# Performance work log

Measured on AMD Instinct MI355X. Metric: run time of the kernel, lower is better.

## Reference

```python
import jax, jax.numpy as jnp
import numpy as np

N = 4_194_304
B = 64
H = 16
TAU = 1.0


def setup_inputs() -> dict:
    key = jax.random.key(0)
    ks = jax.random.split(key, 8)
    pos = jax.random.normal(ks[0], (N, 3), dtype=jnp.float32)
    reflectance = jax.random.uniform(ks[1], (N,), dtype=jnp.float32)
    batch = jnp.sort(jax.random.randint(ks[2], (N,), 0, B).astype(jnp.int32))
    gumbels = jax.random.gumbel(ks[3], (B, 2), dtype=jnp.float32)
    W1 = jax.random.normal(ks[4], (4, H), dtype=jnp.float32) * 0.5
    b1 = jnp.zeros((H,), dtype=jnp.float32)
    W2 = jax.random.normal(ks[5], (H, H), dtype=jnp.float32) * 0.25
    b2 = jnp.zeros((H,), dtype=jnp.float32)
    Wg = jax.random.normal(ks[6], (H, 2), dtype=jnp.float32) * 0.25
    bg = jnp.array([0.0, 2.0], dtype=jnp.float32)  # gate_nn bias init per module
    return {"pos": pos, "reflectance": reflectance, "batch": batch, "gumbels": gumbels,
            "W1": W1, "b1": b1, "W2": W2, "b2": b2, "Wg": Wg, "bg": bg}


def reference(pos, reflectance, batch, gumbels, W1, b1, W2, b2, Wg, bg):
    # point-wise MLP: [N,4] -> [N,H]
    features = jnp.concatenate([pos, reflectance[:, None]], axis=-1)
    h = jax.nn.relu(features @ W1 + b1)
    h = jax.nn.relu(h @ W2 + b2)
    # batch-indexed max pool: [N,H] -> [B,H]
    sample_features = jax.ops.segment_max(h, batch, num_segments=B)
    gate_logits = sample_features @ Wg + bg  # [B,2]
    # gumbel-softmax (hard=False as in forward)
    gate_decision = jax.nn.softmax((gate_logits + gumbels) / TAU, axis=-1)
    # gather per-point gate and scale reflectance
    use_reflectance = gate_decision[:, 1][batch]  # [N]
    return use_reflectance * reflectance
```

## Files before the change

kernel.cpp:

```cpp
#include <hip/hip_runtime.h>
#include <hip/hip_bf16.h>


#define N_PTS 4194304
#define NB 64
#define NH 16
#define WPB 4
#define SITERS 2
#define PTW (256 * SITERS)
#define PPB (WPB * PTW)
#define NBLK (N_PTS / PPB)
#define NENT (NBLK * 2)

typedef __attribute__((ext_vector_type(8))) short bf16x8;
typedef __attribute__((ext_vector_type(4))) float f32x4;
union U8 { bf16x8 v; unsigned u[4]; unsigned short s[8]; };

struct Rec { int idA, idB, bpos; };
struct F3  { float x, y, z; };

__device__ __forceinline__ unsigned pk2(float a, float b) {
    float2 t; t.x = a; t.y = b;
    __hip_bfloat162 r = __float22bfloat162_rn(t);
    unsigned u;
    __builtin_memcpy(&u, &r, sizeof(u));
    return u;
}
__device__ __forceinline__ unsigned short f2bf(float x) {
    unsigned u = __float_as_uint(x);
    u = u + 0x7fffu + ((u >> 16) & 1u);
    return (unsigned short)(u >> 16);
}

template<bool SLOW>
__device__ __forceinline__ void do_chunk(
    const F3 p[4], const float4& rv,
    int sb, int g, int col, int bposw,
    const U8& A1, const U8& A2, const f32x4& c1, const f32x4& c2,
    f32x4& accA, f32x4& accB)
{
    const float f[4][4] = {{p[0].x, p[0].y, p[0].z, rv.x},
                           {p[1].x, p[1].y, p[1].z, rv.y},
                           {p[2].x, p[2].y, p[2].z, rv.z},
                           {p[3].x, p[3].y, p[3].z, rv.w}};
#pragma unroll
    for (int j = 0; j < 4; ++j) {
        const unsigned F01 = pk2(f[j][0], f[j][1]);
        const unsigned F23 = pk2(f[j][2], f[j][3]);
        f32x4 d[4], h[4];
#pragma unroll
        for (int t = 0; t < 4; ++t) {
            const bool mine = (g == t);
            U8 B;
            B.u[0] = mine ? F01 : 0u;
            B.u[1] = mine ? F23 : 0u;
            B.u[2] = 0u; B.u[3] = 0u;
            d[t] = __builtin_amdgcn_mfma_f32_16x16x32_bf16(A1.v, B.v, c1, 0, 0, 0);
        }
#pragma unroll
        for (int t = 0; t < 4; ++t) {
            U8 P;
            P.u[0] = pk2(fmaxf(d[t][0], 0.f), fmaxf(d[t][1], 0.f));
            P.u[1] = pk2(fmaxf(d[t][2], 0.f), fmaxf(d[t][3], 0.f));
            P.u[2] = 0u; P.u[3] = 0u;
            h[t] = __builtin_amdgcn_mfma_f32_16x16x32_bf16(A2.v, P.v, c2, 0, 0, 0);
        }
#pragma unroll
        for (int t = 0; t < 4; ++t) {
            if (!SLOW) {
#pragma unroll
                for (int r = 0; r < 4; ++r) accA[r] = fmaxf(accA[r], h[t][r]);
            } else {
                const bool m = (sb + 64 * j + 16 * t + col) < bposw;
#pragma unroll
                for (int r = 0; r < 4; ++r) {
                    accA[r] = fmaxf(accA[r], m ? h[t][r] : 0.f);
                    accB[r] = fmaxf(accB[r], m ? 0.f : h[t][r]);
                }
            }
        }
    }
}

__global__ __launch_bounds__(256, 8) void mlp_segmax_kernel(
    const float* __restrict__ pos,
    const float* __restrict__ refl,
    const int*   __restrict__ batch,
    const float* __restrict__ W1, const float* __restrict__ b1,
    const float* __restrict__ W2, const float* __restrict__ b2,
    float* __restrict__ pv,
    int*   __restrict__ pid,
    Rec*   __restrict__ recs)
{
    __shared__ float wlds[352];
    __shared__ float lv[WPB][2][NH];
    __shared__ int   li[WPB][2];
    __shared__ int   lbp[WPB];

    const int tid  = threadIdx.x;
    const int lane = tid & 63;
    const int wid  = tid >> 6;
    const int col  = lane & 15;
    const int g    = lane >> 4;
    const int wb   = (blockIdx.x * WPB + wid) * PTW;

    if (tid < 64)  wlds[tid]        = W1[tid];
    if (tid < 16)  wlds[64 + tid]   = b1[tid];
    wlds[80 + tid] = W2[tid];
    if (tid < 16)  wlds[336 + tid]  = b2[tid];
    __syncthreads();

    U8 A1, A2;
#pragma unroll
    for (int e = 0; e < 4; ++e) {
        A1.s[e]     = f2bf(wlds[e * NH + col]);
        A1.s[e + 4] = 0;
        A2.s[e]     = f2bf(wlds[80 + (4 * g + e) * NH + col]);
        A2.s[e + 4] = 0;
    }
    f32x4 c1, c2;
#pragma unroll
    for (int r = 0; r < 4; ++r) {
        c1[r] = wlds[64 + 4 * g + r];
        c2[r] = wlds[336 + 4 * g + r];
    }

    const int idA = batch[wb];
    const int idB = batch[wb + PTW - 1];
    const bool isSlow = (idA != idB);

    f32x4 accA = {0.f, 0.f, 0.f, 0.f};
    f32x4 accB = {0.f, 0.f, 0.f, 0.f};

    if (!isSlow) {
#pragma unroll
        for (int s = 0; s < SITERS; ++s) {
            const int sb = wb + s * 256;
            const float* pb = pos + (size_t)sb * 3;
            const float* rb = refl + sb;
            F3 p[4];
            __builtin_memcpy(&p[0], pb + 3 * (0 * 64 + lane), 12);
            __builtin_memcpy(&p[1], pb + 3 * (1 * 64 + lane), 12);
            __builtin_memcpy(&p[2], pb + 3 * (2 * 64 + lane), 12);
            __builtin_memcpy(&p[3], pb + 3 * (3 * 64 + lane), 12);
            float4 rv;
            rv.x = rb[0 * 64 + lane];
            rv.y = rb[1 * 64 + lane];
            rv.z = rb[2 * 64 + lane];
            rv.w = rb[3 * 64 + lane];
            do_chunk<false>(p, rv, sb, g, col, 0,
                            A1, A2, c1, c2, accA, accB);
        }
    } else {
        int bposw = 0x7fffffff;
        for (int it = 0; it < PTW / 64; ++it) {
            const int idx = wb + it * 64 + lane;
            const unsigned long long mk = __ballot(batch[idx] != idA);
            if (mk) bposw = min(bposw, wb + it * 64 + (__ffsll((long long)mk) - 1));
        }
#pragma unroll
        for (int s = 0; s < SITERS; ++s) {
            const int sb = wb + s * 256;
            const float* pb = pos + (size_t)sb * 3;
            const float* rb = refl + sb;
            F3 p[4];
            __builtin_memcpy(&p[0], pb + 3 * (0 * 64 + lane), 12);
            __builtin_memcpy(&p[1], pb + 3 * (1 * 64 + lane), 12);
            __builtin_memcpy(&p[2], pb + 3 * (2 * 64 + lane), 12);
            __builtin_memcpy(&p[3], pb + 3 * (3 * 64 + lane), 12);
            float4 rv;
            rv.x = rb[0 * 64 + lane];
            rv.y = rb[1 * 64 + lane];
            rv.z = rb[2 * 64 + lane];
            rv.w = rb[3 * 64 + lane];
            do_chunk<true>(p, rv, sb, g, col, bposw,
                           A1, A2, c1, c2, accA, accB);
        }
        lbp[wid] = bposw;
    }

#pragma unroll
    for (int mk = 1; mk <= 8; mk <<= 1) {
#pragma unroll
        for (int r = 0; r < 4; ++r) {
            accA[r] = fmaxf(accA[r], __shfl_xor(accA[r], mk));
            accB[r] = fmaxf(accB[r], __shfl_xor(accB[r], mk));
        }
    }
    if (col == 0) {
        *reinterpret_cast<float4*>(&lv[wid][0][4 * g]) =
            make_float4(accA[0], accA[1], accA[2], accA[3]);
        *reinterpret_cast<float4*>(&lv[wid][1][4 * g]) =
            make_float4(accB[0], accB[1], accB[2], accB[3]);
    }
    if (lane == 0) {
        li[wid][0] = idA; li[wid][1] = idB;
        if (!isSlow) lbp[wid] = 0x7fffffff;
    }
    __syncthreads();

    if (tid < NH) {
        const int d   = tid;
        const int ida = li[0][0];
        const int idb = li[WPB - 1][1];
        float mA = 0.f, mB = 0.f;
#pragma unroll
        for (int s = 0; s < WPB; ++s)
#pragma unroll
            for (int hh = 0; hh < 2; ++hh) {
                const float val = lv[s][hh][d];
                if (li[s][hh] == ida) mA = fmaxf(mA, val);
                else                  mB = fmaxf(mB, val);
            }
        pv[(blockIdx.x * 2 + 0) * NH + d] = mA;
        pv[(blockIdx.x * 2 + 1) * NH + d] = mB;
        if (d == 0) {
            pid[blockIdx.x * 2 + 0] = ida;
            pid[blockIdx.x * 2 + 1] = idb;
            int bp = 0x7fffffff;
#pragma unroll
            for (int s = 0; s < WPB; ++s) {
                if (li[s][0] != ida) bp = min(bp, (int)(blockIdx.x * PPB + s * PTW));
                else if (lbp[s] != 0x7fffffff) bp = min(bp, lbp[s]);
            }
            Rec r; r.idA = ida; r.idB = idb; r.bpos = bp;
            recs[blockIdx.x] = r;
        }
    }
}

__global__ __launch_bounds__(256) void gate_scale_kernel(
    const float* __restrict__ refl,
    const float* __restrict__ pv,
    const int*   __restrict__ pid,
    const Rec*   __restrict__ recs,
    const float* __restrict__ Wg, const float* __restrict__ bg,
    const float* __restrict__ gum,
    float* __restrict__ out)
{
    __shared__ unsigned smA[NH], smB[NH];
    __shared__ unsigned short list[256];
    __shared__ unsigned cnt;
    __shared__ float gAB[2];

    const int tid = threadIdx.x;
    const Rec rec = recs[blockIdx.x >> 1];

    if (tid < NH) { smA[tid] = 0u; smB[tid] = 0u; }
    if (tid == 0) cnt = 0u;
    __syncthreads();

#pragma unroll
    for (int k = 0; k < NENT / 256; ++k) {
        const int e = k * 256 + tid;
        const int p = pid[e];
        const bool a = (p == rec.idA);
        const bool b = (p == rec.idB) && !a;
        if (a || b) {
            const unsigned i = atomicAdd(&cnt, 1u);
            if (i < 256u) list[i] = (unsigned short)(e | (a ? 0 : 0x8000));
        }
    }
    __syncthreads();

    const int n = (int)(cnt < 256u ? cnt : 256u);
    for (int k = tid; k < n * NH; k += 256) {
        const int i = k >> 4, d = k & 15;
        const int e = list[i] & 0x7fff;
        unsigned* dst = (list[i] & 0x8000) ? smB : smA;
        atomicMax(dst + d, __float_as_uint(pv[e * NH + d]));
    }
    __syncthreads();

    if (tid < 2) {
        const int bsel = tid ? rec.idB : rec.idA;
        const unsigned* sm = tid ? smB : smA;
        float l0 = bg[0] + gum[bsel * 2 + 0];
        float l1 = bg[1] + gum[bsel * 2 + 1];
#pragma unroll
        for (int k = 0; k < NH; ++k) {
            const float s = __uint_as_float(sm[k]);
            l0 = fmaf(s, Wg[k * 2 + 0], l0);
            l1 = fmaf(s, Wg[k * 2 + 1], l1);
        }
        gAB[tid] = 1.f / (1.f + expf(-(l1 - l0)));
    }
    __syncthreads();

    const float gA = gAB[0];
    const float gB = (rec.idA == rec.idB) ? gAB[0] : gAB[1];

    const int p0 = (blockIdx.x * 256 + tid) * 4;
    const float4 rv = *reinterpret_cast<const float4*>(refl + p0);
    float4 o;
    o.x = ((p0 + 0) < rec.bpos ? gA : gB) * rv.x;
    o.y = ((p0 + 1) < rec.bpos ? gA : gB) * rv.y;
    o.z = ((p0 + 2) < rec.bpos ? gA : gB) * rv.z;
    o.w = ((p0 + 3) < rec.bpos ? gA : gB) * rv.w;
    *reinterpret_cast<float4*>(out + p0) = o;
}

extern "C" void kernel_launch(void* const* d_in, const int* in_sizes, int n_in,
                              void* d_out, int out_size, void* d_ws, size_t ws_size,
                              hipStream_t stream) {
    const float* pos   = (const float*)d_in[0];
    const float* refl  = (const float*)d_in[1];
    const int*   batch = (const int*)d_in[2];
    const float* gumb  = (const float*)d_in[3];
    const float* W1    = (const float*)d_in[4];
    const float* b1    = (const float*)d_in[5];
    const float* W2    = (const float*)d_in[6];
    const float* b2    = (const float*)d_in[7];
    const float* Wg    = (const float*)d_in[8];
    const float* bg    = (const float*)d_in[9];
    float* out = (float*)d_out;

    float* pv   = (float*)d_ws;
    int*   pid  = (int*)((char*)d_ws + 262144);
    Rec*   recs = (Rec*)((char*)d_ws + 278528);

    mlp_segmax_kernel<<<NBLK, 256, 0, stream>>>(pos, refl, batch,
                                                W1, b1, W2, b2, pv, pid, recs);
    gate_scale_kernel<<<N_PTS / 1024, 256, 0, stream>>>(refl, pv, pid, recs,
                                                        Wg, bg, gumb, out);
}
```

Before: 43.17 us.

## Halve points per MLP block and have each gate block cover two MLP records

The MLP/segment-max kernel now processes 256 points per wavefront instead of 512, which doubles its grid to 4096 blocks and the partial-max entries to 8192. The gate/scale kernel now handles 2048 points per block, merging two consecutive block records and recomputing the segment boundary, and its list capacity grows to 384. The intent is more parallelism in the first kernel, at the cost of the gate kernel scanning twice as many partial entries per block. Workspace offsets are moved to fit the larger partial arrays.

```diff
diff --git a/kernel.cpp b/kernel.cpp
--- a/kernel.cpp
+++ b/kernel.cpp
@@ -6,11 +6,13 @@
 #define NB 64
 #define NH 16
 #define WPB 4
-#define SITERS 2
+#define SITERS 1
 #define PTW (256 * SITERS)
 #define PPB (WPB * PTW)
 #define NBLK (N_PTS / PPB)
 #define NENT (NBLK * 2)
+#define BPPB 2048
+#define NBBLK (N_PTS / BPPB)
 
 typedef __attribute__((ext_vector_type(8))) short bf16x8;
 typedef __attribute__((ext_vector_type(4))) float f32x4;
@@ -132,50 +134,40 @@
     f32x4 accA = {0.f, 0.f, 0.f, 0.f};
     f32x4 accB = {0.f, 0.f, 0.f, 0.f};
 
+    const float* pb = pos + (size_t)wb * 3;
+    const float* rb = refl + wb;
+
     if (!isSlow) {
-#pragma unroll
-        for (int s = 0; s < SITERS; ++s) {
-            const int sb = wb + s * 256;
-            const float* pb = pos + (size_t)sb * 3;
-            const float* rb = refl + sb;
-            F3 p[4];
-            __builtin_memcpy(&p[0], pb + 3 * (0 * 64 + lane), 12);
-            __builtin_memcpy(&p[1], pb + 3 * (1 * 64 + lane), 12);
-            __builtin_memcpy(&p[2], pb + 3 * (2 * 64 + lane), 12);
-            __builtin_memcpy(&p[3], pb + 3 * (3 * 64 + lane), 12);
-            float4 rv;
-            rv.x = rb[0 * 64 + lane];
-            rv.y = rb[1 * 64 + lane];
-            rv.z = rb[2 * 64 + lane];
-            rv.w = rb[3 * 64 + lane];
-            do_chunk<false>(p, rv, sb, g, col, 0,
-                            A1, A2, c1, c2, accA, accB);
-        }
+        F3 p[4];
+        __builtin_memcpy(&p[0], pb + 3 * (0 * 64 + lane), 12);
+        __builtin_memcpy(&p[1], pb + 3 * (1 * 64 + lane), 12);
+        __builtin_memcpy(&p[2], pb + 3 * (2 * 64 + lane), 12);
+        __builtin_memcpy(&p[3], pb + 3 * (3 * 64 + lane), 12);
+        float4 rv;
+        rv.x = rb[0 * 64 + lane];
+        rv.y = rb[1 * 64 + lane];
+        rv.z = rb[2 * 64 + lane];
+        rv.w = rb[3 * 64 + lane];
+        do_chunk<false>(p, rv, wb, g, col, 0, A1, A2, c1, c2, accA, accB);
     } else {
         int bposw = 0x7fffffff;
+#pragma unroll
         for (int it = 0; it < PTW / 64; ++it) {
             const int idx = wb + it * 64 + lane;
             const unsigned long long mk = __ballot(batch[idx] != idA);
             if (mk) bposw = min(bposw, wb + it * 64 + (__ffsll((long long)mk) - 1));
         }
-#pragma unroll
-        for (int s = 0; s < SITERS; ++s) {
-            const int sb = wb + s * 256;
-            const float* pb = pos + (size_t)sb * 3;
-            const float* rb = refl + sb;
-            F3 p[4];
-            __builtin_memcpy(&p[0], pb + 3 * (0 * 64 + lane), 12);
-            __builtin_memcpy(&p[1], pb + 3 * (1 * 64 + lane), 12);
-            __builtin_memcpy(&p[2], pb + 3 * (2 * 64 + lane), 12);
-            __builtin_memcpy(&p[3], pb + 3 * (3 * 64 + lane), 12);
-            float4 rv;
-            rv.x = rb[0 * 64 + lane];
-            rv.y = rb[1 * 64 + lane];
-            rv.z = rb[2 * 64 + lane];
-            rv.w = rb[3 * 64 + lane];
-            do_chunk<true>(p, rv, sb, g, col, bposw,
-                           A1, A2, c1, c2, accA, accB);
-        }
+        F3 p[4];
+        __builtin_memcpy(&p[0], pb + 3 * (0 * 64 + lane), 12);
+        __builtin_memcpy(&p[1], pb + 3 * (1 * 64 + lane), 12);
+        __builtin_memcpy(&p[2], pb + 3 * (2 * 64 + lane), 12);
+        __builtin_memcpy(&p[3], pb + 3 * (3 * 64 + lane), 12);
+        float4 rv;
+        rv.x = rb[0 * 64 + lane];
+        rv.y = rb[1 * 64 + lane];
+        rv.z = rb[2 * 64 + lane];
+        rv.w = rb[3 * 64 + lane];
+        do_chunk<true>(p, rv, wb, g, col, bposw, A1, A2, c1, c2, accA, accB);
         lbp[wid] = bposw;
     }
 
@@ -239,31 +231,36 @@
     float* __restrict__ out)
 {
     __shared__ unsigned smA[NH], smB[NH];
-    __shared__ unsigned short list[256];
+    __shared__ unsigned short list[384];
     __shared__ unsigned cnt;
     __shared__ float gAB[2];
 
     const int tid = threadIdx.x;
-    const Rec rec = recs[blockIdx.x >> 1];
+    const Rec r0 = recs[blockIdx.x * 2 + 0];
+    const Rec r1 = recs[blockIdx.x * 2 + 1];
+    const int idA = r0.idA;
+    const int idB = r1.idB;
+    int bp = min(r0.bpos, r1.bpos);
+    if (r0.idB != r1.idA) bp = min(bp, (int)(blockIdx.x * BPPB + BPPB / 2));
 
     if (tid < NH) { smA[tid] = 0u; smB[tid] = 0u; }
     if (tid == 0) cnt = 0u;
     __syncthreads();
 
-#pragma unroll
+#pragma unroll 8
     for (int k = 0; k < NENT / 256; ++k) {
         const int e = k * 256 + tid;
         const int p = pid[e];
-        const bool a = (p == rec.idA);
-        const bool b = (p == rec.idB) && !a;
+        const bool a = (p == idA);
+        const bool b = (p == idB) && !a;
         if (a || b) {
             const unsigned i = atomicAdd(&cnt, 1u);
-            if (i < 256u) list[i] = (unsigned short)(e | (a ? 0 : 0x8000));
-        }
-    }
-    __syncthreads();
-
-    const int n = (int)(cnt < 256u ? cnt : 256u);
+            if (i < 384u) list[i] = (unsigned short)(e | (a ? 0 : 0x8000));
+        }
+    }
+    __syncthreads();
+
+    const int n = (int)(cnt < 384u ? cnt : 384u);
     for (int k = tid; k < n * NH; k += 256) {
         const int i = k >> 4, d = k & 15;
         const int e = list[i] & 0x7fff;
@@ -273,7 +270,7 @@
     __syncthreads();
 
     if (tid < 2) {
-        const int bsel = tid ? rec.idB : rec.idA;
+        const int bsel = tid ? idB : idA;
         const unsigned* sm = tid ? smB : smA;
         float l0 = bg[0] + gum[bsel * 2 + 0];
         float l1 = bg[1] + gum[bsel * 2 + 1];
@@ -288,16 +285,19 @@
     __syncthreads();
 
     const float gA = gAB[0];
-    const float gB = (rec.idA == rec.idB) ? gAB[0] : gAB[1];
-
-    const int p0 = (blockIdx.x * 256 + tid) * 4;
-    const float4 rv = *reinterpret_cast<const float4*>(refl + p0);
-    float4 o;
-    o.x = ((p0 + 0) < rec.bpos ? gA : gB) * rv.x;
-    o.y = ((p0 + 1) < rec.bpos ? gA : gB) * rv.y;
-    o.z = ((p0 + 2) < rec.bpos ? gA : gB) * rv.z;
-    o.w = ((p0 + 3) < rec.bpos ? gA : gB) * rv.w;
-    *reinterpret_cast<float4*>(out + p0) = o;
+    const float gB = (idA == idB) ? gAB[0] : gAB[1];
+
+#pragma unroll
+    for (int k = 0; k < 2; ++k) {
+        const int p0 = blockIdx.x * BPPB + (k * 256 + tid) * 4;
+        const float4 rv = *reinterpret_cast<const float4*>(refl + p0);
+        float4 o;
+        o.x = ((p0 + 0) < bp ? gA : gB) * rv.x;
+        o.y = ((p0 + 1) < bp ? gA : gB) * rv.y;
+        o.z = ((p0 + 2) < bp ? gA : gB) * rv.z;
+        o.w = ((p0 + 3) < bp ? gA : gB) * rv.w;
+        *reinterpret_cast<float4*>(out + p0) = o;
+    }
 }
 
 extern "C" void kernel_launch(void* const* d_in, const int* in_sizes, int n_in,
@@ -316,11 +316,11 @@
     float* out = (float*)d_out;
 
     float* pv   = (float*)d_ws;
-    int*   pid  = (int*)((char*)d_ws + 262144);
-    Rec*   recs = (Rec*)((char*)d_ws + 278528);
+    int*   pid  = (int*)((char*)d_ws + 524288);
+    Rec*   recs = (Rec*)((char*)d_ws + 524288 + 32768);
 
     mlp_segmax_kernel<<<NBLK, 256, 0, stream>>>(pos, refl, batch,
                                                 W1, b1, W2, b2, pv, pid, recs);
-    gate_scale_kernel<<<N_PTS / 1024, 256, 0, stream>>>(refl, pv, pid, recs,
-                                                        Wg, bg, gumb, out);
-}
+    gate_scale_kernel<<<NBBLK, 256, 0, stream>>>(refl, pv, pid, recs,
+                                                 Wg, bg, gumb, out);
+}
```

New measurement: 43.83 us. Within noise of the previous version (+1.5%).
